# Optimization experiments

Measured on AMD Instinct MI355X. Metric: run time of the kernel, lower is better.

## Reference

```python
import jax, jax.numpy as jnp
import numpy as np

N, F, H, O = 3072, 128, 16, 8  # nodes, in_channels, hidden_channels, out_channels


def setup_inputs() -> dict:
    key = jax.random.key(0)
    ks = jax.random.split(key, 8)
    s = 0.01  # xavier gain=0.01 in original init -> small weights
    return {
        "x": jax.random.normal(ks[0], (N, F), dtype=jnp.float32),
        "edge_index": jax.random.randint(ks[1], (2, N * 32), 0, N, dtype=jnp.int64),
        "node_distances": jax.random.uniform(ks[2], (N, N), dtype=jnp.float32),
        "normalization_matrix": jnp.ones((N, N), dtype=jnp.float32),
        # per-feature MLPs fs[f]: Linear(1,H) -> ReLU -> (Dropout p=0) -> Linear(H,O), stacked over F
        "W1": s * jax.random.normal(ks[3], (F, H), dtype=jnp.float32),
        "b1": jnp.zeros((F, H), dtype=jnp.float32),
        "W2": s * jax.random.normal(ks[4], (F, H, O), dtype=jnp.float32),
        "b2": jnp.zeros((F, O), dtype=jnp.float32),
        # rho MLP: Linear(1,H) -> ReLU -> Linear(H,O) (bias=True since is_graph_task=False)
        "rW1": s * jax.random.normal(ks[5], (H,), dtype=jnp.float32),
        "rb1": jnp.zeros((H,), dtype=jnp.float32),
        "rW2": s * jax.random.normal(ks[6], (H, O), dtype=jnp.float32),
        "rb2": jnp.zeros((O,), dtype=jnp.float32),
    }


def reference(x, edge_index, node_distances, normalization_matrix,
              W1, b1, W2, b2, rW1, rb1, rW2, rb2):
    # --- per-feature tiny MLPs, vectorized over the feature axis ---
    # h[n,f,:] = relu(x[n,f] * W1[f] + b1[f])
    h = jax.nn.relu(x[:, :, None] * W1[None, :, :] + b1[None, :, :])  # [N,F,H]
    fx = jnp.einsum('nfh,fho->nfo', h, W2) + b2[None, :, :]           # [N,F,O]
    # sum over features first (commutes with the matmul's F-reduction)
    g = fx.sum(axis=1)                                                 # [N,O]

    # --- rho MLP on normalized pairwise distances ---
    d = node_distances / normalization_matrix                          # [N,N]
    hd = jax.nn.relu(d[:, :, None] * rW1 + rb1)                        # [N,N,H]
    m = jnp.einsum('nmh,ho->nmo', hd, rW2) + rb2                       # [N,N,O]

    # out.T in torch: mf = m_dist_perm @ fx_perm summed over features -> [N,O]
    out = jnp.einsum('nmo,mo->no', m, g)                               # [N,O]
    return out
```

## Files before the change

### kernel.cpp

```cpp
#include <hip/hip_runtime.h>
#include <hip/hip_bf16.h>

#define NN 3072
#define FF 128
#define HH 16
#define OO 8

#define NODES_PER_BLOCK 8

__global__ __launch_bounds__(128) void gnan_g_kernel(
    const float* __restrict__ x,
    const float* __restrict__ W1,
    const float* __restrict__ b1,
    const float* __restrict__ W2,
    const float* __restrict__ b2,
    float* __restrict__ g)
{
    const int f  = threadIdx.x;
    const int n0 = blockIdx.x * NODES_PER_BLOCK;

    float w1[HH], bb1[HH], w2[HH][OO], bb2[OO];
#pragma unroll
    for (int h = 0; h < HH; ++h) {
        w1[h]  = W1[f * HH + h];
        bb1[h] = b1[f * HH + h];
    }
#pragma unroll
    for (int h = 0; h < HH; ++h)
#pragma unroll
        for (int o = 0; o < OO; ++o)
            w2[h][o] = W2[(f * HH + h) * OO + o];
#pragma unroll
    for (int o = 0; o < OO; ++o) bb2[o] = b2[f * OO + o];

    __shared__ float wsum[2][OO];

    for (int ni = 0; ni < NODES_PER_BLOCK; ++ni) {
        const int n = n0 + ni;
        const float xv = x[(size_t)n * FF + f];

        float v[OO];
#pragma unroll
        for (int o = 0; o < OO; ++o) v[o] = bb2[o];
#pragma unroll
        for (int h = 0; h < HH; ++h) {
            float a = fmaxf(xv * w1[h] + bb1[h], 0.f);
#pragma unroll
            for (int o = 0; o < OO; ++o) v[o] += a * w2[h][o];
        }

#pragma unroll
        for (int o = 0; o < OO; ++o) {
#pragma unroll
            for (int off = 32; off > 0; off >>= 1)
                v[o] += __shfl_down(v[o], off);
        }
        const int lane = threadIdx.x & 63;
        const int wid  = threadIdx.x >> 6;
        if (lane == 0) {
#pragma unroll
            for (int o = 0; o < OO; ++o) wsum[wid][o] = v[o];
        }
        __syncthreads();
        if (threadIdx.x < OO) {
            g[(size_t)n * OO + threadIdx.x] =
                wsum[0][threadIdx.x] + wsum[1][threadIdx.x];
        }
        __syncthreads();
    }
}

__global__ __launch_bounds__(256) void gnan_main_kernel(
    const float* __restrict__ nd,
    const float* __restrict__ nm,
    const float* __restrict__ g,
    const float* __restrict__ rW1,
    const float* __restrict__ rb1,
    const float* __restrict__ rW2,
    const float* __restrict__ rb2,
    float* __restrict__ out)
{
    const int n = blockIdx.x;
    const int t = threadIdx.x;

    float w1[HH], bb1[HH], w2[HH][OO], bb2[OO];
#pragma unroll
    for (int h = 0; h < HH; ++h) { w1[h] = rW1[h]; bb1[h] = rb1[h]; }
#pragma unroll
    for (int h = 0; h < HH; ++h)
#pragma unroll
        for (int o = 0; o < OO; ++o) w2[h][o] = rW2[h * OO + o];
#pragma unroll
    for (int o = 0; o < OO; ++o) bb2[o] = rb2[o];

    const float* __restrict__ drow = nd + (size_t)n * NN;
    const float* __restrict__ nrow = nm + (size_t)n * NN;

    float acc[OO];
#pragma unroll
    for (int o = 0; o < OO; ++o) acc[o] = 0.f;

    for (int m = t; m < NN; m += 256) {
        const float dv = __fdividef(drow[m], nrow[m]);
        const float4 g0 = *reinterpret_cast<const float4*>(g + (size_t)m * OO);
        const float4 g1 = *reinterpret_cast<const float4*>(g + (size_t)m * OO + 4);

        float a[HH];
#pragma unroll
        for (int h = 0; h < HH; ++h)
            a[h] = fmaxf(dv * w1[h] + bb1[h], 0.f);

        float v[OO];
#pragma unroll
        for (int o = 0; o < OO; ++o) v[o] = bb2[o];
#pragma unroll
        for (int h = 0; h < HH; ++h)
#pragma unroll
            for (int o = 0; o < OO; ++o)
                v[o] += a[h] * w2[h][o];

        acc[0] += v[0] * g0.x;
        acc[1] += v[1] * g0.y;
        acc[2] += v[2] * g0.z;
        acc[3] += v[3] * g0.w;
        acc[4] += v[4] * g1.x;
        acc[5] += v[5] * g1.y;
        acc[6] += v[6] * g1.z;
        acc[7] += v[7] * g1.w;
    }

#pragma unroll
    for (int o = 0; o < OO; ++o) {
#pragma unroll
        for (int off = 32; off > 0; off >>= 1)
            acc[o] += __shfl_down(acc[o], off);
    }
    __shared__ float wsum[4][OO];
    const int lane = t & 63;
    const int wid  = t >> 6;
    if (lane == 0) {
#pragma unroll
        for (int o = 0; o < OO; ++o) wsum[wid][o] = acc[o];
    }
    __syncthreads();
    if (t < OO) {
        out[(size_t)n * OO + t] =
            wsum[0][t] + wsum[1][t] + wsum[2][t] + wsum[3][t];
    }
}

extern "C" void kernel_launch(void* const* d_in, const int* in_sizes, int n_in,
                              void* d_out, int out_size, void* d_ws, size_t ws_size,
                              hipStream_t stream) {
    const float* x   = (const float*)d_in[0];
    const float* nd  = (const float*)d_in[2];
    const float* nm  = (const float*)d_in[3];
    const float* W1  = (const float*)d_in[4];
    const float* b1  = (const float*)d_in[5];
    const float* W2  = (const float*)d_in[6];
    const float* b2  = (const float*)d_in[7];
    const float* rW1 = (const float*)d_in[8];
    const float* rb1 = (const float*)d_in[9];
    const float* rW2 = (const float*)d_in[10];
    const float* rb2 = (const float*)d_in[11];
    float* out = (float*)d_out;

    float* g = (float*)d_ws;

    gnan_g_kernel<<<NN / NODES_PER_BLOCK, 128, 0, stream>>>(x, W1, b1, W2, b2, g);
    gnan_main_kernel<<<NN, 256, 0, stream>>>(nd, nm, g, rW1, rb1, rW2, rb2, out);
}
```

Measured before the change: 177.9 us.

## Replace rho MLP with piecewise-linear lookup and stage transposed g in LDS

Rewrites the distance MLP as a piecewise-linear function of d: the ReLU breakpoints are sorted once per block, and per-segment slope/intercept coefficients are precomputed, so each element costs a segment check and eight FMAs instead of a 16x8 MLP. g is written transposed and the whole 96KB array is copied into shared memory for each block. Each wave now handles one row, with 12 rows per 768-thread block. This removes most of the ALU work, but adds a per-block staging copy of g, divergent segment lookups, and high LDS use that limits occupancy.

New measurement: 152.6 us. -14.2%, faster.

```diff
diff --git a/kernel.cpp b/kernel.cpp
--- a/kernel.cpp
+++ b/kernel.cpp
@@ -1,12 +1,13 @@
 #include <hip/hip_runtime.h>
 #include <hip/hip_bf16.h>
+#include <math.h>
 
 #define NN 3072
 #define FF 128
 #define HH 16
 #define OO 8
 
-#define NODES_PER_BLOCK 8
+#define NPB 4
 
 __global__ __launch_bounds__(128) void gnan_g_kernel(
     const float* __restrict__ x,
@@ -14,10 +15,10 @@
     const float* __restrict__ b1,
     const float* __restrict__ W2,
     const float* __restrict__ b2,
-    float* __restrict__ g)
+    float* __restrict__ gT)
 {
     const int f  = threadIdx.x;
-    const int n0 = blockIdx.x * NODES_PER_BLOCK;
+    const int n0 = blockIdx.x * NPB;
 
     float w1[HH], bb1[HH], w2[HH][OO], bb2[OO];
 #pragma unroll
@@ -35,7 +36,7 @@
 
     __shared__ float wsum[2][OO];
 
-    for (int ni = 0; ni < NODES_PER_BLOCK; ++ni) {
+    for (int ni = 0; ni < NPB; ++ni) {
         const int n = n0 + ni;
         const float xv = x[(size_t)n * FF + f];
 
@@ -63,70 +64,128 @@
         }
         __syncthreads();
         if (threadIdx.x < OO) {
-            g[(size_t)n * OO + threadIdx.x] =
-                wsum[0][threadIdx.x] + wsum[1][threadIdx.x];
+            gT[threadIdx.x * NN + n] = wsum[0][threadIdx.x] + wsum[1][threadIdx.x];
         }
         __syncthreads();
     }
 }
 
-__global__ __launch_bounds__(256) void gnan_main_kernel(
+__global__ __launch_bounds__(768) void gnan_main_kernel(
     const float* __restrict__ nd,
     const float* __restrict__ nm,
-    const float* __restrict__ g,
+    const float* __restrict__ gT,
     const float* __restrict__ rW1,
     const float* __restrict__ rb1,
     const float* __restrict__ rW2,
     const float* __restrict__ rb2,
     float* __restrict__ out)
 {
-    const int n = blockIdx.x;
+    __shared__ float gs[OO * NN];
+    __shared__ float Kp[HH + 2];
+    __shared__ float rowsA[HH + 1][16];
+    __shared__ float sk[HH];
+    __shared__ int   shh[HH];
+    __shared__ float cAdd[OO];
+
     const int t = threadIdx.x;
 
-    float w1[HH], bb1[HH], w2[HH][OO], bb2[OO];
-#pragma unroll
-    for (int h = 0; h < HH; ++h) { w1[h] = rW1[h]; bb1[h] = rb1[h]; }
-#pragma unroll
-    for (int h = 0; h < HH; ++h)
-#pragma unroll
-        for (int o = 0; o < OO; ++o) w2[h][o] = rW2[h * OO + o];
-#pragma unroll
-    for (int o = 0; o < OO; ++o) bb2[o] = rb2[o];
-
-    const float* __restrict__ drow = nd + (size_t)n * NN;
-    const float* __restrict__ nrow = nm + (size_t)n * NN;
+    if (t == 0) {
+        for (int h = 0; h < HH; ++h) {
+            float w = rW1[h];
+            sk[h]  = (w != 0.0f) ? (-rb1[h] / w) : INFINITY;
+            shh[h] = h;
+        }
+        for (int i = 1; i < HH; ++i) {
+            float kv = sk[i]; int iv = shh[i];
+            int p = i - 1;
+            while (p >= 0 && sk[p] > kv) { sk[p+1]=sk[p]; shh[p+1]=shh[p]; --p; }
+            sk[p+1] = kv; shh[p+1] = iv;
+        }
+        Kp[0] = -INFINITY;
+        for (int h = 0; h < HH; ++h) Kp[h + 1] = sk[h];
+        Kp[HH + 1] = INFINITY;
+    }
+    if (t < OO) {
+        float c = rb2[t];
+        for (int h = 0; h < HH; ++h)
+            if (rW1[h] == 0.0f) c += fmaxf(rb1[h], 0.f) * rW2[h * OO + t];
+        cAdd[t] = c;
+    }
+    __syncthreads();
+    if (t < (HH + 1) * OO) {
+        const int j = t >> 3, o = t & 7;
+        float alpha = 0.f, beta = 0.f;
+        for (int p = 0; p < HH; ++p) {
+            const int h = shh[p];
+            const float w = rW1[h];
+            const bool active = (w > 0.f) ? (p < j) : (w < 0.f ? (p >= j) : false);
+            if (active) {
+                alpha += w       * rW2[h * OO + o];
+                beta  += rb1[h]  * rW2[h * OO + o];
+            }
+        }
+        rowsA[j][o]     = alpha;
+        rowsA[j][8 + o] = beta + cAdd[o];
+    }
+
+    {
+        float4*       dst = reinterpret_cast<float4*>(gs);
+        const float4* src = reinterpret_cast<const float4*>(gT);
+        for (int i = t; i < OO * NN / 4; i += 768) dst[i] = src[i];
+    }
+    __syncthreads();
+
+    const int wave = t >> 6;
+    const int lane = t & 63;
+    const int row  = blockIdx.x * 12 + wave;
+
+    const float* __restrict__ drow = nd + (size_t)row * NN;
+    const float* __restrict__ nrow = nm + (size_t)row * NN;
+
+    float CA[OO], CB[OO];
+    float clo = INFINITY, chi = -INFINITY;
+#pragma unroll
+    for (int o = 0; o < OO; ++o) { CA[o] = 0.f; CB[o] = 0.f; }
 
     float acc[OO];
 #pragma unroll
     for (int o = 0; o < OO; ++o) acc[o] = 0.f;
 
-    for (int m = t; m < NN; m += 256) {
-        const float dv = __fdividef(drow[m], nrow[m]);
-        const float4 g0 = *reinterpret_cast<const float4*>(g + (size_t)m * OO);
-        const float4 g1 = *reinterpret_cast<const float4*>(g + (size_t)m * OO + 4);
-
-        float a[HH];
-#pragma unroll
-        for (int h = 0; h < HH; ++h)
-            a[h] = fmaxf(dv * w1[h] + bb1[h], 0.f);
-
-        float v[OO];
-#pragma unroll
-        for (int o = 0; o < OO; ++o) v[o] = bb2[o];
-#pragma unroll
-        for (int h = 0; h < HH; ++h)
-#pragma unroll
-            for (int o = 0; o < OO; ++o)
-                v[o] += a[h] * w2[h][o];
-
-        acc[0] += v[0] * g0.x;
-        acc[1] += v[1] * g0.y;
-        acc[2] += v[2] * g0.z;
-        acc[3] += v[3] * g0.w;
-        acc[4] += v[4] * g1.x;
-        acc[5] += v[5] * g1.y;
-        acc[6] += v[6] * g1.z;
-        acc[7] += v[7] * g1.w;
+    for (int it = 0; it < NN / 128; ++it) {
+        const int m0 = it * 128 + lane * 2;
+        const float2 dv2 = *reinterpret_cast<const float2*>(drow + m0);
+        const float2 nv2 = *reinterpret_cast<const float2*>(nrow + m0);
+
+        float2 gv[OO];
+#pragma unroll
+        for (int o = 0; o < OO; ++o)
+            gv[o] = *reinterpret_cast<const float2*>(&gs[o * NN + m0]);
+
+#pragma unroll
+        for (int k = 0; k < 2; ++k) {
+            const float d = __fdividef(k == 0 ? dv2.x : dv2.y,
+                                       k == 0 ? nv2.x : nv2.y);
+            if (d < clo || d >= chi) {
+                int j = 0;
+#pragma unroll
+                for (int p = 0; p < HH; ++p) j += (d >= Kp[p + 1]) ? 1 : 0;
+                clo = Kp[j];
+                chi = Kp[j + 1];
+                const float4 a0 = *reinterpret_cast<const float4*>(&rowsA[j][0]);
+                const float4 a1 = *reinterpret_cast<const float4*>(&rowsA[j][4]);
+                const float4 b0 = *reinterpret_cast<const float4*>(&rowsA[j][8]);
+                const float4 b1 = *reinterpret_cast<const float4*>(&rowsA[j][12]);
+                CA[0]=a0.x; CA[1]=a0.y; CA[2]=a0.z; CA[3]=a0.w;
+                CA[4]=a1.x; CA[5]=a1.y; CA[6]=a1.z; CA[7]=a1.w;
+                CB[0]=b0.x; CB[1]=b0.y; CB[2]=b0.z; CB[3]=b0.w;
+                CB[4]=b1.x; CB[5]=b1.y; CB[6]=b1.z; CB[7]=b1.w;
+            }
+#pragma unroll
+            for (int o = 0; o < OO; ++o) {
+                const float g = (k == 0) ? gv[o].x : gv[o].y;
+                acc[o] = fmaf(fmaf(CA[o], d, CB[o]), g, acc[o]);
+            }
+        }
     }
 
 #pragma unroll
@@ -135,17 +194,10 @@
         for (int off = 32; off > 0; off >>= 1)
             acc[o] += __shfl_down(acc[o], off);
     }
-    __shared__ float wsum[4][OO];
-    const int lane = t & 63;
-    const int wid  = t >> 6;
     if (lane == 0) {
 #pragma unroll
-        for (int o = 0; o < OO; ++o) wsum[wid][o] = acc[o];
-    }
-    __syncthreads();
-    if (t < OO) {
-        out[(size_t)n * OO + t] =
-            wsum[0][t] + wsum[1][t] + wsum[2][t] + wsum[3][t];
+        for (int o = 0; o < OO; ++o)
+            out[(size_t)row * OO + o] = acc[o];
     }
 }
 
@@ -165,8 +217,8 @@
     const float* rb2 = (const float*)d_in[11];
     float* out = (float*)d_out;
 
-    float* g = (float*)d_ws;
-
-    gnan_g_kernel<<<NN / NODES_PER_BLOCK, 128, 0, stream>>>(x, W1, b1, W2, b2, g);
-    gnan_main_kernel<<<NN, 256, 0, stream>>>(nd, nm, g, rW1, rb1, rW2, rb2, out);
+    float* gT = (float*)d_ws;
+
+    gnan_g_kernel<<<NN / NPB, 128, 0, stream>>>(x, W1, b1, W2, b2, gT);
+    gnan_main_kernel<<<NN / 12, 768, 0, stream>>>(nd, nm, gT, rW1, rb1, rW2, rb2, out);
 }
```
